# Performance work log

Measured on AMD Instinct MI355X. Metric: run time of the kernel, lower is better.

The kernel has to match this reference:

```python
import jax, jax.numpy as jnp
import numpy as np
from jax.scipy.special import logsumexp

# Module hyperparameters
N_PARTS = 128
BATCH = 1024
# Entropic-regularized solver settings (differentiable surrogate for the
# cvxpylayers LP solve; eps small relative to O(1) eta-phi distances)
EPS = 0.02
ITERS = 100
LOG_FLOOR = 1e-30  # avoid log(0) for zero-mass dummy particles


def setup_inputs() -> dict:
    key = jax.random.key(0)
    k1, k2 = jax.random.split(key)
    # [B, n_parts, 3]: features (eta, phi, pt); uniform fill keeps pt > 0
    jets1 = jax.random.uniform(k1, (BATCH, N_PARTS, 3), dtype=jnp.float32)
    jets2 = jax.random.uniform(k2, (BATCH, N_PARTS, 3), dtype=jnp.float32)
    return {"jets1": jets1, "jets2": jets2}


def _sinkhorn_flow(C, loga, logb):
    """Batched log-domain Sinkhorn. C: [B,N,M], loga: [B,N], logb: [B,M].
    Returns the transport plan (flow) [B,N,M] with marginals ~ (a, b)."""
    f = jnp.zeros_like(loga)
    g = jnp.zeros_like(logb)

    def step(carry, _):
        f, g = carry
        f = EPS * (loga - logsumexp((g[:, None, :] - C) / EPS, axis=2))
        g = EPS * (logb - logsumexp((f[:, :, None] - C) / EPS, axis=1))
        return (f, g), None

    (f, g), _ = jax.lax.scan(step, (f, g), None, length=ITERS)
    return jnp.exp((f[:, :, None] + g[:, None, :] - C) / EPS)


def reference(jets1, jets2):
    n = jets1.shape[1]
    # Pairwise eta-phi ground distances: [B, n, n]
    diffs = -(jets1[:, :, None, :2] - jets2[:, None, :, :2]) + 1e-12
    dists = jnp.linalg.norm(diffs, axis=3)
    # pt weights (LP marginals)
    w1 = jets1[:, :, 2]
    w2 = jets2[:, :, 2]
    E1 = jnp.sum(w1, axis=1)
    E2 = jnp.sum(w2, axis=1)
    EabsDiff = jnp.abs(E2 - E1)
    # Partial OT (total mass = min(E1,E2), row/col sums <= w) is made balanced
    # by adding one zero-cost dummy particle per side absorbing the excess mass.
    a = jnp.concatenate([w1, jnp.maximum(E2 - E1, 0.0)[:, None]], axis=1)  # [B, n+1]
    b = jnp.concatenate([w2, jnp.maximum(E1 - E2, 0.0)[:, None]], axis=1)  # [B, n+1]
    Cp = jnp.pad(dists, ((0, 0), (0, 1), (0, 1)))  # dummy row/col have zero cost
    loga = jnp.log(jnp.maximum(a, LOG_FLOOR))
    logb = jnp.log(jnp.maximum(b, LOG_FLOOR))
    flow = _sinkhorn_flow(Cp, loga, logb)  # [B, n+1, n+1]
    # EMD = transport cost over real particles + energy-difference penalty
    emds = jnp.sum(dists * flow[:, :n, :n], axis=(1, 2)) + EabsDiff  # [B]
    return emds
```

## Files before the change

kernel.cpp:

```cpp
#include <hip/hip_runtime.h>

#define NP    128
#define NITER 100
#define RSC   72.13475204444817f
#define IRSC  0.013862943611198906f

typedef __attribute__((ext_vector_type(8))) short bf16x8;
typedef __attribute__((ext_vector_type(4))) float f32x4;

__device__ __forceinline__ float wsum64(float x) {
  #pragma unroll
  for (int s = 1; s < 64; s <<= 1) x += __shfl_xor(x, s);
  return x;
}
__device__ __forceinline__ float bf2f(unsigned short h) {
  return __uint_as_float(((unsigned)h) << 16);
}
__device__ __forceinline__ unsigned short f2bf(float f) {
  unsigned u = __float_as_uint(f);
  u += 0x7fffu + ((u >> 16) & 1u);
  return (unsigned short)(u >> 16);
}

__global__ __launch_bounds__(128, 2) void emd_sinkhorn(
    const float* __restrict__ j1g, const float* __restrict__ j2g,
    float* __restrict__ out)
{
  __shared__ __align__(16) float x1s[NP], y1s[NP], x2s[NP], y2s[NP];
  __shared__ __align__(16) float ahs[NP], bhs[NP];
  __shared__ __align__(16) float Slds[NP];
  __shared__ __align__(16) float Tlds[NP];
  __shared__ float red[2];

  const int t  = threadIdx.x;
  const int l  = t & 63;
  const int wv = t >> 6;
  const int lg = l >> 4;
  const int li = l & 15;
  const int b  = blockIdx.x;
  const float* J1 = j1g + (size_t)b * (NP * 3);
  const float* J2 = j2g + (size_t)b * (NP * 3);

  if (t < NP) {
    x1s[t] = J1[3*t]; y1s[t] = J1[3*t+1]; ahs[t] = J1[3*t+2];
    x2s[t] = J2[3*t]; y2s[t] = J2[3*t+1]; bhs[t] = J2[3*t+2];
  }
  __syncthreads();

  const float e1 = wsum64(ahs[l] + ahs[l + 64]);
  const float e2 = wsum64(bhs[l] + bhs[l + 64]);
  const float dE = fabsf(e2 - e1);
  const float aslk = fmaxf(fmaxf(e2 - e1, 0.0f), 1e-30f);
  const float bslk = fmaxf(fmaxf(e1 - e2, 0.0f), 1e-30f);
  const float2 araw = *(const float2*)&ahs[2*l];
  const float2 braw = *(const float2*)&bhs[2*l];
  const float ah0 = fmaxf(araw.x, 1e-30f), ah1 = fmaxf(araw.y, 1e-30f);
  const float bh0 = fmaxf(braw.x, 1e-30f), bh1 = fmaxf(braw.y, 1e-30f);

  bf16x8 KA[4][4], KB[4][4];
  #pragma unroll
  for (int rt = 0; rt < 4; ++rt) {
    const int n = 64*wv + 16*rt + li;
    const float xr = x1s[n], yr = y1s[n];
    #pragma unroll
    for (int kt = 0; kt < 4; ++kt) {
      #pragma unroll
      for (int i2 = 0; i2 < 8; ++i2) {
        const int k = 32*kt + 8*lg + i2;
        const float dx = x2s[k] - xr + 1e-12f;
        const float dy = y2s[k] - yr + 1e-12f;
        KA[rt][kt][i2] = (short)f2bf(
            __builtin_amdgcn_exp2f(-__builtin_sqrtf(dx*dx + dy*dy) * RSC));
      }
    }
  }
  #pragma unroll
  for (int ct = 0; ct < 4; ++ct) {
    const int m = 64*wv + 16*ct + li;
    const float xc = x2s[m], yc = y2s[m];
    #pragma unroll
    for (int kt = 0; kt < 4; ++kt) {
      #pragma unroll
      for (int i2 = 0; i2 < 8; ++i2) {
        const int k = 32*kt + 8*lg + i2;
        const float dx = xc - x1s[k] + 1e-12f;
        const float dy = yc - y1s[k] + 1e-12f;
        KB[ct][kt][i2] = (short)f2bf(
            __builtin_amdgcn_exp2f(-__builtin_sqrtf(dx*dx + dy*dy) * RSC));
      }
    }
  }

  unsigned Qpk = 0x3F803F80u;
  unsigned Ppk = 0;
  float SQ = 128.0f, q128 = 1.0f;

  for (int it = 0; it < NITER; ++it) {
    const float p128 = aslk * __builtin_amdgcn_rcpf(SQ + q128);

    bf16x8 qf[4];
    #pragma unroll
    for (int kt = 0; kt < 4; ++kt) {
      union { unsigned u[4]; bf16x8 v; } r;
      #pragma unroll
      for (int q = 0; q < 4; ++q)
        r.u[q] = (unsigned)__builtin_amdgcn_ds_bpermute(
            4*(16*kt + 4*lg + q), (int)Qpk);
      qf[kt] = r.v;
    }

    f32x4 acc[4];
    #pragma unroll
    for (int rt = 0; rt < 4; ++rt) {
      acc[rt] = (f32x4){q128, q128, q128, q128};
      #pragma unroll
      for (int kt = 0; kt < 4; ++kt)
        acc[rt] = __builtin_amdgcn_mfma_f32_16x16x32_bf16(
            KA[rt][kt], qf[kt], acc[rt], 0, 0, 0);
    }
    if (li == 0) {
      #pragma unroll
      for (int rt = 0; rt < 4; ++rt)
        *(f32x4*)&Slds[64*wv + 16*rt + 4*lg] = acc[rt];
    }
    __syncthreads();

    const float2 s2 = *(const float2*)&Slds[2*l];
    const float P0 = ah0 * __builtin_amdgcn_rcpf(s2.x);
    const float P1 = ah1 * __builtin_amdgcn_rcpf(s2.y);
    const float SP = wsum64(P0 + P1);
    const float q128n = bslk * __builtin_amdgcn_rcpf(SP + p128);
    Ppk = (unsigned)f2bf(P0) | ((unsigned)f2bf(P1) << 16);

    bf16x8 pf[4];
    #pragma unroll
    for (int kt = 0; kt < 4; ++kt) {
      union { unsigned u[4]; bf16x8 v; } r;
      #pragma unroll
      for (int q = 0; q < 4; ++q)
        r.u[q] = (unsigned)__builtin_amdgcn_ds_bpermute(
            4*(16*kt + 4*lg + q), (int)Ppk);
      pf[kt] = r.v;
    }

    f32x4 acc2[4];
    #pragma unroll
    for (int ct = 0; ct < 4; ++ct) {
      acc2[ct] = (f32x4){p128, p128, p128, p128};
      #pragma unroll
      for (int kt = 0; kt < 4; ++kt)
        acc2[ct] = __builtin_amdgcn_mfma_f32_16x16x32_bf16(
            pf[kt], KB[ct][kt], acc2[ct], 0, 0, 0);
    }
    if (lg == 0) {
      #pragma unroll
      for (int ct = 0; ct < 4; ++ct)
        Tlds[64*wv + 16*ct + li] = acc2[ct][0];
    }
    __syncthreads();

    const float2 t2 = *(const float2*)&Tlds[2*l];
    const float Q0 = bh0 * __builtin_amdgcn_rcpf(t2.x);
    const float Q1 = bh1 * __builtin_amdgcn_rcpf(t2.y);
    SQ = wsum64(Q0 + Q1);
    Qpk = (unsigned)f2bf(Q0) | ((unsigned)f2bf(Q1) << 16);
    q128 = q128n;
  }

  bf16x8 qf[4];
  #pragma unroll
  for (int kt = 0; kt < 4; ++kt) {
    union { unsigned u[4]; bf16x8 v; } r;
    #pragma unroll
    for (int q = 0; q < 4; ++q)
      r.u[q] = (unsigned)__builtin_amdgcn_ds_bpermute(
          4*(16*kt + 4*lg + q), (int)Qpk);
    qf[kt] = r.v;
  }
  float accE = 0.0f;
  #pragma unroll
  for (int rt = 0; rt < 4; ++rt) {
    const int n = 64*wv + 16*rt + li;
    const unsigned pr = (unsigned)__builtin_amdgcn_ds_bpermute(
        4*(n >> 1), (int)Ppk);
    const float Pn = bf2f((unsigned short)((li & 1) ? (pr >> 16) : pr));
    #pragma unroll
    for (int kt = 0; kt < 4; ++kt) {
      #pragma unroll
      for (int i2 = 0; i2 < 8; ++i2) {
        const float kk = bf2f((unsigned short)KA[rt][kt][i2]);
        const float qm = bf2f((unsigned short)qf[kt][i2]);
        const float d  = -__builtin_amdgcn_logf(kk) * IRSC;
        accE = fmaf(d, (Pn * kk) * qm, accE);
      }
    }
  }
  accE = wsum64(accE);
  if (l == 0) red[wv] = accE;
  __syncthreads();
  if (t == 0) out[b] = (red[0] + red[1]) + dE;
}

extern "C" void kernel_launch(void* const* d_in, const int* in_sizes, int n_in,
                              void* d_out, int out_size, void* d_ws, size_t ws_size,
                              hipStream_t stream) {
  const float* j1 = (const float*)d_in[0];
  const float* j2 = (const float*)d_in[1];
  float* outp = (float*)d_out;
  const int batch = in_sizes[0] / (NP * 3);
  hipLaunchKernelGGL(emd_sinkhorn, dim3(batch), dim3(128), 0, stream,
                     j1, j2, outp);
}
```

Baseline: 232.9 us.

## Split Sinkhorn block across four waves and compute marginal sums via ones-MFMA

Doubles the block from two waves to four, so each wave holds half as many kernel tiles and runs half as many MFMAs per half-iteration. The dummy-particle normalization sums, previously computed with wavefront shuffle reductions, now come from an extra MFMA against a ones vector inside the matrix-vector product. This shortens the serial per-iteration dependency chain and cuts register pressure. The cost is more waves contending at each barrier and an extra MFMA per product. The sums also pass through bf16 inputs and use a different summation order.

```diff
diff --git a/kernel.cpp b/kernel.cpp
--- a/kernel.cpp
+++ b/kernel.cpp
@@ -22,7 +22,7 @@
   return (unsigned short)(u >> 16);
 }
 
-__global__ __launch_bounds__(128, 2) void emd_sinkhorn(
+__global__ __launch_bounds__(256, 2) void emd_sinkhorn(
     const float* __restrict__ j1g, const float* __restrict__ j2g,
     float* __restrict__ out)
 {
@@ -30,7 +30,7 @@
   __shared__ __align__(16) float ahs[NP], bhs[NP];
   __shared__ __align__(16) float Slds[NP];
   __shared__ __align__(16) float Tlds[NP];
-  __shared__ float red[2];
+  __shared__ float red[4];
 
   const int t  = threadIdx.x;
   const int l  = t & 63;
@@ -57,10 +57,10 @@
   const float ah0 = fmaxf(araw.x, 1e-30f), ah1 = fmaxf(araw.y, 1e-30f);
   const float bh0 = fmaxf(braw.x, 1e-30f), bh1 = fmaxf(braw.y, 1e-30f);
 
-  bf16x8 KA[4][4], KB[4][4];
-  #pragma unroll
-  for (int rt = 0; rt < 4; ++rt) {
-    const int n = 64*wv + 16*rt + li;
+  bf16x8 KA[2][4], KB[2][4];
+  #pragma unroll
+  for (int rt = 0; rt < 2; ++rt) {
+    const int n = 32*wv + 16*rt + li;
     const float xr = x1s[n], yr = y1s[n];
     #pragma unroll
     for (int kt = 0; kt < 4; ++kt) {
@@ -75,8 +75,8 @@
     }
   }
   #pragma unroll
-  for (int ct = 0; ct < 4; ++ct) {
-    const int m = 64*wv + 16*ct + li;
+  for (int ct = 0; ct < 2; ++ct) {
+    const int m = 32*wv + 16*ct + li;
     const float xc = x2s[m], yc = y2s[m];
     #pragma unroll
     for (int kt = 0; kt < 4; ++kt) {
@@ -91,13 +91,15 @@
     }
   }
 
+  bf16x8 onef;
+  #pragma unroll
+  for (int i2 = 0; i2 < 8; ++i2) onef[i2] = (short)0x3F80;
+
   unsigned Qpk = 0x3F803F80u;
   unsigned Ppk = 0;
-  float SQ = 128.0f, q128 = 1.0f;
+  float q128 = 1.0f;
 
   for (int it = 0; it < NITER; ++it) {
-    const float p128 = aslk * __builtin_amdgcn_rcpf(SQ + q128);
-
     bf16x8 qf[4];
     #pragma unroll
     for (int kt = 0; kt < 4; ++kt) {
@@ -109,27 +111,26 @@
       qf[kt] = r.v;
     }
 
-    f32x4 acc[4];
-    #pragma unroll
-    for (int rt = 0; rt < 4; ++rt) {
-      acc[rt] = (f32x4){q128, q128, q128, q128};
-      #pragma unroll
-      for (int kt = 0; kt < 4; ++kt)
-        acc[rt] = __builtin_amdgcn_mfma_f32_16x16x32_bf16(
-            KA[rt][kt], qf[kt], acc[rt], 0, 0, 0);
-    }
+    f32x4 acc[2], accS;
+    accS = (f32x4){q128, q128, q128, q128};
+    #pragma unroll
+    for (int rt = 0; rt < 2; ++rt) acc[rt] = (f32x4){q128, q128, q128, q128};
+    #pragma unroll
+    for (int kt = 0; kt < 4; ++kt) {
+      acc[0] = __builtin_amdgcn_mfma_f32_16x16x32_bf16(KA[0][kt], qf[kt], acc[0], 0, 0, 0);
+      acc[1] = __builtin_amdgcn_mfma_f32_16x16x32_bf16(KA[1][kt], qf[kt], acc[1], 0, 0, 0);
+      accS   = __builtin_amdgcn_mfma_f32_16x16x32_bf16(onef, qf[kt], accS, 0, 0, 0);
+    }
+    const float p128 = aslk * __builtin_amdgcn_rcpf(accS[0]);
     if (li == 0) {
-      #pragma unroll
-      for (int rt = 0; rt < 4; ++rt)
-        *(f32x4*)&Slds[64*wv + 16*rt + 4*lg] = acc[rt];
+      *(f32x4*)&Slds[32*wv + 4*lg]      = acc[0];
+      *(f32x4*)&Slds[32*wv + 16 + 4*lg] = acc[1];
     }
     __syncthreads();
 
     const float2 s2 = *(const float2*)&Slds[2*l];
     const float P0 = ah0 * __builtin_amdgcn_rcpf(s2.x);
     const float P1 = ah1 * __builtin_amdgcn_rcpf(s2.y);
-    const float SP = wsum64(P0 + P1);
-    const float q128n = bslk * __builtin_amdgcn_rcpf(SP + p128);
     Ppk = (unsigned)f2bf(P0) | ((unsigned)f2bf(P1) << 16);
 
     bf16x8 pf[4];
@@ -143,28 +144,27 @@
       pf[kt] = r.v;
     }
 
-    f32x4 acc2[4];
-    #pragma unroll
-    for (int ct = 0; ct < 4; ++ct) {
-      acc2[ct] = (f32x4){p128, p128, p128, p128};
-      #pragma unroll
-      for (int kt = 0; kt < 4; ++kt)
-        acc2[ct] = __builtin_amdgcn_mfma_f32_16x16x32_bf16(
-            pf[kt], KB[ct][kt], acc2[ct], 0, 0, 0);
-    }
+    f32x4 acc2[2], accS2;
+    accS2 = (f32x4){p128, p128, p128, p128};
+    #pragma unroll
+    for (int ct = 0; ct < 2; ++ct) acc2[ct] = (f32x4){p128, p128, p128, p128};
+    #pragma unroll
+    for (int kt = 0; kt < 4; ++kt) {
+      acc2[0] = __builtin_amdgcn_mfma_f32_16x16x32_bf16(pf[kt], KB[0][kt], acc2[0], 0, 0, 0);
+      acc2[1] = __builtin_amdgcn_mfma_f32_16x16x32_bf16(pf[kt], KB[1][kt], acc2[1], 0, 0, 0);
+      accS2   = __builtin_amdgcn_mfma_f32_16x16x32_bf16(pf[kt], onef, accS2, 0, 0, 0);
+    }
+    q128 = bslk * __builtin_amdgcn_rcpf(accS2[0]);
     if (lg == 0) {
-      #pragma unroll
-      for (int ct = 0; ct < 4; ++ct)
-        Tlds[64*wv + 16*ct + li] = acc2[ct][0];
+      Tlds[32*wv + li]      = acc2[0][0];
+      Tlds[32*wv + 16 + li] = acc2[1][0];
     }
     __syncthreads();
 
     const float2 t2 = *(const float2*)&Tlds[2*l];
     const float Q0 = bh0 * __builtin_amdgcn_rcpf(t2.x);
     const float Q1 = bh1 * __builtin_amdgcn_rcpf(t2.y);
-    SQ = wsum64(Q0 + Q1);
     Qpk = (unsigned)f2bf(Q0) | ((unsigned)f2bf(Q1) << 16);
-    q128 = q128n;
   }
 
   bf16x8 qf[4];
@@ -179,8 +179,8 @@
   }
   float accE = 0.0f;
   #pragma unroll
-  for (int rt = 0; rt < 4; ++rt) {
-    const int n = 64*wv + 16*rt + li;
+  for (int rt = 0; rt < 2; ++rt) {
+    const int n = 32*wv + 16*rt + li;
     const unsigned pr = (unsigned)__builtin_amdgcn_ds_bpermute(
         4*(n >> 1), (int)Ppk);
     const float Pn = bf2f((unsigned short)((li & 1) ? (pr >> 16) : pr));
@@ -198,7 +198,7 @@
   accE = wsum64(accE);
   if (l == 0) red[wv] = accE;
   __syncthreads();
-  if (t == 0) out[b] = (red[0] + red[1]) + dE;
+  if (t == 0) out[b] = ((red[0] + red[1]) + (red[2] + red[3])) + dE;
 }
 
 extern "C" void kernel_launch(void* const* d_in, const int* in_sizes, int n_in,
@@ -208,6 +208,6 @@
   const float* j2 = (const float*)d_in[1];
   float* outp = (float*)d_out;
   const int batch = in_sizes[0] / (NP * 3);
-  hipLaunchKernelGGL(emd_sinkhorn, dim3(batch), dim3(128), 0, stream,
+  hipLaunchKernelGGL(emd_sinkhorn, dim3(batch), dim3(256), 0, stream,
                      j1, j2, outp);
 }
```

Result: no change. 230.1 us (-1.2%).
